# Optimization experiments

Measured on AMD Instinct MI355X. Metric: run time of the kernel, lower is better.

## Reference

```python
import jax, jax.numpy as jnp
import numpy as np

EPS = 1e-05


def setup_inputs() -> dict:
    key = jax.random.key(0)
    ks = jax.random.split(key, 4)
    B, N, D, H, E = 16, 8192, 128, 64, 64
    x = jax.random.normal(ks[0], (B, N, D), dtype=jnp.float32)
    ln_w = jnp.ones((D,), jnp.float32)
    ln_b = jnp.zeros((D,), jnp.float32)
    Wl = jax.random.normal(ks[1], (D, H), dtype=jnp.float32) / np.sqrt(D)
    bl = jnp.zeros((H,), jnp.float32)
    Wr = jax.random.normal(ks[2], (D, H), dtype=jnp.float32) / np.sqrt(D)
    br = jnp.zeros((H,), jnp.float32)
    Wo = jax.random.normal(ks[3], (H, E), dtype=jnp.float32) / np.sqrt(H)
    bo = jnp.zeros((E,), jnp.float32)
    return {"x": x, "ln_w": ln_w, "ln_b": ln_b, "Wl": Wl, "bl": bl,
            "Wr": Wr, "br": br, "Wo": Wo, "bo": bo}


def _layernorm(x, w, b):
    mu = jnp.mean(x, axis=-1, keepdims=True)
    var = jnp.mean(jnp.square(x - mu), axis=-1, keepdims=True)
    return (x - mu) * jax.lax.rsqrt(var + EPS) * w + b


def reference(x, ln_w, ln_b, Wl, bl, Wr, br, Wo, bo):
    # x: [B, N, D]
    xn = _layernorm(x, ln_w, ln_b)
    left = xn @ Wl + bl    # [B, N, H]
    right = xn @ Wr + br   # [B, N, H]
    # Original: einsum('b i d, b j d -> b i j d').mean(dim=1).
    # Identical math without the O(N^2) tensor: mean over i factors out of
    # the product since left[b,i,d]*right[b,j,d] is separable in i.
    outer = left.mean(axis=1)[:, None, :] * right  # [B, N, H]
    return outer @ Wo + bo  # [B, N, E]
```

## Files before the change

### kernel.cpp

```cpp
#include <hip/hip_runtime.h>
#include <math.h>

#define B_  16
#define N_  8192
#define D_  128
#define H_  64
#define E_  64
#define EPSLN 1e-5f

typedef __attribute__((ext_vector_type(8))) short short8;
typedef __attribute__((ext_vector_type(4))) float f32x4;

#define WSB_COL 0
#define WSB_MT  8192
#define WSB_T   270336
#define WSB_C   274432

static __device__ __forceinline__ unsigned short f2bf(float f) {
    union { float f; unsigned u; } c; c.f = f;
    unsigned u = c.u;
    return (unsigned short)((u + 0x7FFFu + ((u >> 16) & 1u)) >> 16);
}

__global__ __launch_bounds__(256) void k_stats(const float* __restrict__ x,
                                               float* __restrict__ colacc) {
    __shared__ float xs[64 * 132];
    __shared__ float mul[64], rsl[64], red[128];
    int b = blockIdx.y, t = threadIdx.x;
    int rowbase = blockIdx.x * 64;
    size_t gbase = (size_t)(b * N_ + rowbase) * 32;

    const float4* x4 = (const float4*)x;
#pragma unroll
    for (int k = 0; k < 8; ++k) {
        int idx = t + 256 * k;
        int row = idx >> 5, c4 = idx & 31;
        *(float4*)&xs[row * 132 + c4 * 4] = x4[gbase + idx];
    }
    __syncthreads();

    {
        int r = t >> 2, q = t & 3;
        float s = 0.f, s2 = 0.f;
#pragma unroll
        for (int i = 0; i < 8; ++i) {
            float4 v = *(const float4*)&xs[r * 132 + q * 32 + i * 4];
            s  += (v.x + v.y) + (v.z + v.w);
            s2 += (v.x * v.x + v.y * v.y) + (v.z * v.z + v.w * v.w);
        }
        s  += __shfl_xor(s, 1, 64);  s  += __shfl_xor(s, 2, 64);
        s2 += __shfl_xor(s2, 1, 64); s2 += __shfl_xor(s2, 2, 64);
        if (q == 0) {
            float mu  = s * (1.f / D_);
            float var = s2 * (1.f / D_) - mu * mu;
            mul[r] = mu;
            rsl[r] = rsqrtf(var + EPSLN);
        }
    }
    __syncthreads();

    int c = t & 127, hh = t >> 7;
    float acc = 0.f;
#pragma unroll 8
    for (int i = 0; i < 32; ++i) {
        int r = hh * 32 + i;
        acc += rsl[r] * (xs[r * 132 + c] - mul[r]);
    }
    if (hh == 1) red[c] = acc;
    __syncthreads();
    if (hh == 0) atomicAdd(&colacc[b * D_ + c], acc + red[c]);
}

__global__ __launch_bounds__(256) void k_combine(const float* __restrict__ colacc,
                                                 const float* __restrict__ ln_w,
                                                 const float* __restrict__ ln_b,
                                                 const float* __restrict__ Wl,
                                                 const float* __restrict__ bl,
                                                 const float* __restrict__ Wr,
                                                 const float* __restrict__ br,
                                                 const float* __restrict__ Wo,
                                                 const float* __restrict__ bo,
                                                 unsigned short* __restrict__ Mt,
                                                 float* __restrict__ Tg,
                                                 float* __restrict__ Cg) {
    int b = blockIdx.y, dblk = blockIdx.x, t = threadIdx.x;
    __shared__ float cm[D_], ml[H_], uu[H_], qq[H_];
    __shared__ float P[H_ * E_];

    if (t < D_) cm[t] = ln_w[t] * colacc[b * D_ + t] * (1.f / N_) + ln_b[t];
    __syncthreads();

    if (t < H_) {
        float a = bl[t], u = 0.f, q = 0.f;
        for (int d = 0; d < D_; ++d) {
            float wr = Wr[d * H_ + t];
            a += cm[d] * Wl[d * H_ + t];
            u += ln_w[d] * wr;
            q += ln_b[d] * wr;
        }
        ml[t] = a; uu[t] = u; qq[t] = q + br[t];
    }
    __syncthreads();

#pragma unroll
    for (int k = 0; k < 16; ++k) {
        int idx = t + 256 * k;
        P[idx] = ml[idx >> 6] * Wo[idx];
    }
    __syncthreads();

    int d  = dblk * 32 + (t >> 3);
    int eo = (t & 7) * 8;
    float a0 = 0, a1 = 0, a2 = 0, a3 = 0, a4 = 0, a5 = 0, a6 = 0, a7 = 0;
    for (int h = 0; h < H_; ++h) {
        float wr = Wr[d * H_ + h];
        const float4* p4 = (const float4*)&P[h * E_ + eo];
        float4 pa = p4[0], pb = p4[1];
        a0 += wr * pa.x; a1 += wr * pa.y; a2 += wr * pa.z; a3 += wr * pa.w;
        a4 += wr * pb.x; a5 += wr * pb.y; a6 += wr * pb.z; a7 += wr * pb.w;
    }
    float wd = ln_w[d];
    size_t mb = (size_t)b * E_ * D_;
    Mt[mb + (size_t)(eo + 0) * D_ + d] = f2bf(wd * a0);
    Mt[mb + (size_t)(eo + 1) * D_ + d] = f2bf(wd * a1);
    Mt[mb + (size_t)(eo + 2) * D_ + d] = f2bf(wd * a2);
    Mt[mb + (size_t)(eo + 3) * D_ + d] = f2bf(wd * a3);
    Mt[mb + (size_t)(eo + 4) * D_ + d] = f2bf(wd * a4);
    Mt[mb + (size_t)(eo + 5) * D_ + d] = f2bf(wd * a5);
    Mt[mb + (size_t)(eo + 6) * D_ + d] = f2bf(wd * a6);
    Mt[mb + (size_t)(eo + 7) * D_ + d] = f2bf(wd * a7);

    if (dblk == 0 && t < E_) {
        float T = 0.f, C = bo[t];
        for (int h = 0; h < H_; ++h) {
            float p = P[h * E_ + t];
            T += uu[h] * p;
            C += qq[h] * p;
        }
        Tg[b * E_ + t] = T;
        Cg[b * E_ + t] = C;
    }
}

__global__ __launch_bounds__(256, 2) void k_gemm(const float* __restrict__ x,
                                                 const unsigned short* __restrict__ Mt,
                                                 const float* __restrict__ Tg,
                                                 const float* __restrict__ Cg,
                                                 float* __restrict__ out) {
    __shared__ short xs[256 * 128];
    __shared__ float mul[256], rsl[256], Tl[E_], Cl[E_];

    int b = blockIdx.y, t = threadIdx.x;
    int rowbase = blockIdx.x * 256;

    if (t < E_) { Tl[t] = Tg[b * E_ + t]; Cl[t] = Cg[b * E_ + t]; }

    {
        const float4* xrow = (const float4*)(x + (size_t)(b * N_ + rowbase + t) * D_);
        float s = 0.f, s2 = 0.f;
        int sw = t & 15;
#pragma unroll
        for (int g = 0; g < 16; ++g) {
            float4 va = xrow[2 * g], vb = xrow[2 * g + 1];
            s  += (va.x + va.y) + (va.z + va.w) + (vb.x + vb.y) + (vb.z + vb.w);
            s2 += (va.x * va.x + va.y * va.y) + (va.z * va.z + va.w * va.w)
                + (vb.x * vb.x + vb.y * vb.y) + (vb.z * vb.z + vb.w * vb.w);
            short8 sv;
            sv[0] = (short)f2bf(va.x); sv[1] = (short)f2bf(va.y);
            sv[2] = (short)f2bf(va.z); sv[3] = (short)f2bf(va.w);
            sv[4] = (short)f2bf(vb.x); sv[5] = (short)f2bf(vb.y);
            sv[6] = (short)f2bf(vb.z); sv[7] = (short)f2bf(vb.w);
            *(short8*)&xs[t * 128 + ((g ^ sw) * 8)] = sv;
        }
        float mu  = s * (1.f / D_);
        float var = s2 * (1.f / D_) - mu * mu;
        mul[t] = mu;
        rsl[t] = rsqrtf(var + EPSLN);
    }
    __syncthreads();

    int wv = t >> 6, lane = t & 63;
    int m16 = lane & 15, quad = lane >> 4;

    f32x4 acc[4][4];
#pragma unroll
    for (int i = 0; i < 4; ++i)
#pragma unroll
        for (int j = 0; j < 4; ++j) acc[i][j] = (f32x4){0.f, 0.f, 0.f, 0.f};

    const unsigned short* Mb = Mt + (size_t)b * E_ * D_;

#pragma unroll
    for (int kc = 0; kc < 4; ++kc) {
        short8 af[4], bf[4];
#pragma unroll
        for (int mt = 0; mt < 4; ++mt) {
            int row = wv * 64 + mt * 16 + m16;
            int g = kc * 4 + quad;
            af[mt] = *(const short8*)&xs[row * 128 + ((g ^ m16) * 8)];
        }
#pragma unroll
        for (int nt = 0; nt < 4; ++nt) {
            bf[nt] = *(const short8*)(Mb + (size_t)(nt * 16 + m16) * D_ + kc * 32 + quad * 8);
        }
#pragma unroll
        for (int mt = 0; mt < 4; ++mt)
#pragma unroll
            for (int nt = 0; nt < 4; ++nt)
                acc[mt][nt] = __builtin_amdgcn_mfma_f32_16x16x32_bf16(
                    af[mt], bf[nt], acc[mt][nt], 0, 0, 0);
    }

    size_t outbase = (size_t)(b * N_ + rowbase) * E_;
#pragma unroll
    for (int mt = 0; mt < 4; ++mt) {
        int rb = wv * 64 + mt * 16 + quad * 4;
        float mu0 = mul[rb + 0], rs0 = rsl[rb + 0];
        float mu1 = mul[rb + 1], rs1 = rsl[rb + 1];
        float mu2 = mul[rb + 2], rs2 = rsl[rb + 2];
        float mu3 = mul[rb + 3], rs3 = rsl[rb + 3];
#pragma unroll
        for (int nt = 0; nt < 4; ++nt) {
            int col = nt * 16 + m16;
            float Tc = Tl[col], Cc = Cl[col];
            float* o = out + outbase + (size_t)rb * E_ + col;
            o[0 * E_] = rs0 * (acc[mt][nt][0] - mu0 * Tc) + Cc;
            o[1 * E_] = rs1 * (acc[mt][nt][1] - mu1 * Tc) + Cc;
            o[2 * E_] = rs2 * (acc[mt][nt][2] - mu2 * Tc) + Cc;
            o[3 * E_] = rs3 * (acc[mt][nt][3] - mu3 * Tc) + Cc;
        }
    }
}

extern "C" void kernel_launch(void* const* d_in, const int* in_sizes, int n_in,
                              void* d_out, int out_size, void* d_ws, size_t ws_size,
                              hipStream_t stream) {
    const float* x    = (const float*)d_in[0];
    const float* ln_w = (const float*)d_in[1];
    const float* ln_b = (const float*)d_in[2];
    const float* Wl   = (const float*)d_in[3];
    const float* bl   = (const float*)d_in[4];
    const float* Wr   = (const float*)d_in[5];
    const float* br   = (const float*)d_in[6];
    const float* Wo   = (const float*)d_in[7];
    const float* bo   = (const float*)d_in[8];
    float* out = (float*)d_out;
    char* ws   = (char*)d_ws;

    float*          colacc = (float*)(ws + WSB_COL);
    unsigned short* Mt     = (unsigned short*)(ws + WSB_MT);
    float*          Tg     = (float*)(ws + WSB_T);
    float*          Cg     = (float*)(ws + WSB_C);

    hipMemsetAsync(colacc, 0, B_ * D_ * sizeof(float), stream);

    k_stats<<<dim3(N_ / 64, B_), 256, 0, stream>>>(x, colacc);
    k_combine<<<dim3(4, B_), 256, 0, stream>>>(colacc, ln_w, ln_b, Wl, bl, Wr,
                                               br, Wo, bo, Mt, Tg, Cg);
    k_gemm<<<dim3(N_ / 256, B_), 256, 0, stream>>>(x, Mt, Tg, Cg, out);
}
```

Measured before the change: 144.1 us.

## Fuse stats, combine and GEMM into one persistent kernel with grid barriers

Replaces the three-kernel pipeline with a single 256-block kernel that reads x once, converts it to bf16, and keeps one 256-row tile in LDS while spilling the other to a bf16 workspace buffer. Per-block column partials replace the atomic accumulation. Two software grid barriers sequence the weight-combine step and the MFMA GEMM, so x no longer needs a second fp32 read and two launches are removed. The cost is reliance on all 256 blocks being co-resident, a spin barrier with a bailout that could silently break correctness, and column sums now computed from bf16-rounded x.

```diff
diff --git a/kernel.cpp b/kernel.cpp
--- a/kernel.cpp
+++ b/kernel.cpp
@@ -7,179 +7,92 @@
 #define H_  64
 #define E_  64
 #define EPSLN 1e-5f
+#define NBLK 256u
 
 typedef __attribute__((ext_vector_type(8))) short short8;
 typedef __attribute__((ext_vector_type(4))) float f32x4;
 
-#define WSB_COL 0
-#define WSB_MT  8192
-#define WSB_T   270336
-#define WSB_C   274432
+#define WSB_PART 0
+#define WSB_MT   131072
+#define WSB_T    393216
+#define WSB_C    397312
+#define WSB_BAR  401408
+#define WSB_XB   409600
 
 static __device__ __forceinline__ unsigned short f2bf(float f) {
     union { float f; unsigned u; } c; c.f = f;
     unsigned u = c.u;
     return (unsigned short)((u + 0x7FFFu + ((u >> 16) & 1u)) >> 16);
 }
-
-__global__ __launch_bounds__(256) void k_stats(const float* __restrict__ x,
-                                               float* __restrict__ colacc) {
-    __shared__ float xs[64 * 132];
-    __shared__ float mul[64], rsl[64], red[128];
-    int b = blockIdx.y, t = threadIdx.x;
-    int rowbase = blockIdx.x * 64;
-    size_t gbase = (size_t)(b * N_ + rowbase) * 32;
-
-    const float4* x4 = (const float4*)x;
-#pragma unroll
-    for (int k = 0; k < 8; ++k) {
-        int idx = t + 256 * k;
-        int row = idx >> 5, c4 = idx & 31;
-        *(float4*)&xs[row * 132 + c4 * 4] = x4[gbase + idx];
-    }
-    __syncthreads();
-
-    {
-        int r = t >> 2, q = t & 3;
-        float s = 0.f, s2 = 0.f;
-#pragma unroll
-        for (int i = 0; i < 8; ++i) {
-            float4 v = *(const float4*)&xs[r * 132 + q * 32 + i * 4];
-            s  += (v.x + v.y) + (v.z + v.w);
-            s2 += (v.x * v.x + v.y * v.y) + (v.z * v.z + v.w * v.w);
-        }
-        s  += __shfl_xor(s, 1, 64);  s  += __shfl_xor(s, 2, 64);
-        s2 += __shfl_xor(s2, 1, 64); s2 += __shfl_xor(s2, 2, 64);
-        if (q == 0) {
-            float mu  = s * (1.f / D_);
-            float var = s2 * (1.f / D_) - mu * mu;
-            mul[r] = mu;
-            rsl[r] = rsqrtf(var + EPSLN);
-        }
-    }
-    __syncthreads();
-
-    int c = t & 127, hh = t >> 7;
-    float acc = 0.f;
-#pragma unroll 8
-    for (int i = 0; i < 32; ++i) {
-        int r = hh * 32 + i;
-        acc += rsl[r] * (xs[r * 132 + c] - mul[r]);
-    }
-    if (hh == 1) red[c] = acc;
-    __syncthreads();
-    if (hh == 0) atomicAdd(&colacc[b * D_ + c], acc + red[c]);
-}
-
-__global__ __launch_bounds__(256) void k_combine(const float* __restrict__ colacc,
-                                                 const float* __restrict__ ln_w,
-                                                 const float* __restrict__ ln_b,
-                                                 const float* __restrict__ Wl,
-                                                 const float* __restrict__ bl,
-                                                 const float* __restrict__ Wr,
-                                                 const float* __restrict__ br,
-                                                 const float* __restrict__ Wo,
-                                                 const float* __restrict__ bo,
-                                                 unsigned short* __restrict__ Mt,
-                                                 float* __restrict__ Tg,
-                                                 float* __restrict__ Cg) {
-    int b = blockIdx.y, dblk = blockIdx.x, t = threadIdx.x;
-    __shared__ float cm[D_], ml[H_], uu[H_], qq[H_];
-    __shared__ float P[H_ * E_];
-
-    if (t < D_) cm[t] = ln_w[t] * colacc[b * D_ + t] * (1.f / N_) + ln_b[t];
-    __syncthreads();
-
-    if (t < H_) {
-        float a = bl[t], u = 0.f, q = 0.f;
-        for (int d = 0; d < D_; ++d) {
-            float wr = Wr[d * H_ + t];
-            a += cm[d] * Wl[d * H_ + t];
-            u += ln_w[d] * wr;
-            q += ln_b[d] * wr;
-        }
-        ml[t] = a; uu[t] = u; qq[t] = q + br[t];
-    }
-    __syncthreads();
-
-#pragma unroll
-    for (int k = 0; k < 16; ++k) {
-        int idx = t + 256 * k;
-        P[idx] = ml[idx >> 6] * Wo[idx];
-    }
-    __syncthreads();
-
-    int d  = dblk * 32 + (t >> 3);
-    int eo = (t & 7) * 8;
-    float a0 = 0, a1 = 0, a2 = 0, a3 = 0, a4 = 0, a5 = 0, a6 = 0, a7 = 0;
-    for (int h = 0; h < H_; ++h) {
-        float wr = Wr[d * H_ + h];
-        const float4* p4 = (const float4*)&P[h * E_ + eo];
-        float4 pa = p4[0], pb = p4[1];
-        a0 += wr * pa.x; a1 += wr * pa.y; a2 += wr * pa.z; a3 += wr * pa.w;
-        a4 += wr * pb.x; a5 += wr * pb.y; a6 += wr * pb.z; a7 += wr * pb.w;
-    }
-    float wd = ln_w[d];
-    size_t mb = (size_t)b * E_ * D_;
-    Mt[mb + (size_t)(eo + 0) * D_ + d] = f2bf(wd * a0);
-    Mt[mb + (size_t)(eo + 1) * D_ + d] = f2bf(wd * a1);
-    Mt[mb + (size_t)(eo + 2) * D_ + d] = f2bf(wd * a2);
-    Mt[mb + (size_t)(eo + 3) * D_ + d] = f2bf(wd * a3);
-    Mt[mb + (size_t)(eo + 4) * D_ + d] = f2bf(wd * a4);
-    Mt[mb + (size_t)(eo + 5) * D_ + d] = f2bf(wd * a5);
-    Mt[mb + (size_t)(eo + 6) * D_ + d] = f2bf(wd * a6);
-    Mt[mb + (size_t)(eo + 7) * D_ + d] = f2bf(wd * a7);
-
-    if (dblk == 0 && t < E_) {
-        float T = 0.f, C = bo[t];
-        for (int h = 0; h < H_; ++h) {
-            float p = P[h * E_ + t];
-            T += uu[h] * p;
-            C += qq[h] * p;
-        }
-        Tg[b * E_ + t] = T;
-        Cg[b * E_ + t] = C;
-    }
-}
-
-__global__ __launch_bounds__(256, 2) void k_gemm(const float* __restrict__ x,
-                                                 const unsigned short* __restrict__ Mt,
-                                                 const float* __restrict__ Tg,
-                                                 const float* __restrict__ Cg,
-                                                 float* __restrict__ out) {
-    __shared__ short xs[256 * 128];
-    __shared__ float mul[256], rsl[256], Tl[E_], Cl[E_];
-
-    int b = blockIdx.y, t = threadIdx.x;
-    int rowbase = blockIdx.x * 256;
-
-    if (t < E_) { Tl[t] = Tg[b * E_ + t]; Cl[t] = Cg[b * E_ + t]; }
-
-    {
-        const float4* xrow = (const float4*)(x + (size_t)(b * N_ + rowbase + t) * D_);
-        float s = 0.f, s2 = 0.f;
-        int sw = t & 15;
-#pragma unroll
-        for (int g = 0; g < 16; ++g) {
-            float4 va = xrow[2 * g], vb = xrow[2 * g + 1];
-            s  += (va.x + va.y) + (va.z + va.w) + (vb.x + vb.y) + (vb.z + vb.w);
-            s2 += (va.x * va.x + va.y * va.y) + (va.z * va.z + va.w * va.w)
-                + (vb.x * vb.x + vb.y * vb.y) + (vb.z * vb.z + vb.w * vb.w);
-            short8 sv;
-            sv[0] = (short)f2bf(va.x); sv[1] = (short)f2bf(va.y);
-            sv[2] = (short)f2bf(va.z); sv[3] = (short)f2bf(va.w);
-            sv[4] = (short)f2bf(vb.x); sv[5] = (short)f2bf(vb.y);
-            sv[6] = (short)f2bf(vb.z); sv[7] = (short)f2bf(vb.w);
-            *(short8*)&xs[t * 128 + ((g ^ sw) * 8)] = sv;
-        }
-        float mu  = s * (1.f / D_);
-        float var = s2 * (1.f / D_) - mu * mu;
-        mul[t] = mu;
-        rsl[t] = rsqrtf(var + EPSLN);
-    }
-    __syncthreads();
-
-    int wv = t >> 6, lane = t & 63;
+static __device__ __forceinline__ float bf2f(short s) {
+    union { unsigned u; float f; } c;
+    c.u = ((unsigned)(unsigned short)s) << 16;
+    return c.f;
+}
+
+static __device__ __forceinline__ void gridbar(unsigned* bar, unsigned target) {
+    __syncthreads();
+    if (threadIdx.x == 0) {
+        __threadfence();
+        atomicAdd(bar, 1u);
+        int spins = 0;
+        while (atomicAdd(bar, 0u) < target) {
+            __builtin_amdgcn_s_sleep(32);
+            if (++spins > (1 << 15)) break;
+        }
+        __threadfence();
+    }
+    __syncthreads();
+}
+
+static __device__ __forceinline__ void stage_rows(const float* __restrict__ xrows,
+                                                  int t, short* xs,
+                                                  float* muA, float* rsA) {
+    const float4* xrow = (const float4*)(xrows + (size_t)t * D_);
+    float s = 0.f, s2 = 0.f;
+    int sw = t & 15;
+#pragma unroll
+    for (int g = 0; g < 16; ++g) {
+        float4 va = xrow[2 * g], vb = xrow[2 * g + 1];
+        s  += (va.x + va.y) + (va.z + va.w) + (vb.x + vb.y) + (vb.z + vb.w);
+        s2 += (va.x * va.x + va.y * va.y) + (va.z * va.z + va.w * va.w)
+            + (vb.x * vb.x + vb.y * vb.y) + (vb.z * vb.z + vb.w * vb.w);
+        short8 sv;
+        sv[0] = (short)f2bf(va.x); sv[1] = (short)f2bf(va.y);
+        sv[2] = (short)f2bf(va.z); sv[3] = (short)f2bf(va.w);
+        sv[4] = (short)f2bf(vb.x); sv[5] = (short)f2bf(vb.y);
+        sv[6] = (short)f2bf(vb.z); sv[7] = (short)f2bf(vb.w);
+        *(short8*)&xs[t * 128 + ((g ^ sw) * 8)] = sv;
+    }
+    float mu  = s * (1.f / D_);
+    float var = s2 * (1.f / D_) - mu * mu;
+    muA[t] = mu;
+    rsA[t] = rsqrtf(var + EPSLN);
+}
+
+static __device__ __forceinline__ void colsum_pass(const short* xs,
+                                                   const float* muA, const float* rsA,
+                                                   int t, float* ca, float* srm) {
+    int rc = t >> 4, cg = t & 15;
+#pragma unroll
+    for (int i = 0; i < 16; ++i) {
+        int r = rc * 16 + i;
+        float rs = rsA[r];
+        *srm += rs * muA[r];
+        short8 v = *(const short8*)&xs[r * 128 + ((cg ^ (r & 15)) << 3)];
+        ca[0] += rs * bf2f(v[0]); ca[1] += rs * bf2f(v[1]);
+        ca[2] += rs * bf2f(v[2]); ca[3] += rs * bf2f(v[3]);
+        ca[4] += rs * bf2f(v[4]); ca[5] += rs * bf2f(v[5]);
+        ca[6] += rs * bf2f(v[6]); ca[7] += rs * bf2f(v[7]);
+    }
+}
+
+static __device__ __forceinline__ void mfma_tile(const short* xs,
+                                                 const unsigned short* __restrict__ Mb,
+                                                 const float* muA, const float* rsA,
+                                                 const float* Tl, const float* Cl,
+                                                 float* __restrict__ outp,
+                                                 int wv, int lane) {
     int m16 = lane & 15, quad = lane >> 4;
 
     f32x4 acc[4][4];
@@ -187,8 +100,6 @@
     for (int i = 0; i < 4; ++i)
 #pragma unroll
         for (int j = 0; j < 4; ++j) acc[i][j] = (f32x4){0.f, 0.f, 0.f, 0.f};
-
-    const unsigned short* Mb = Mt + (size_t)b * E_ * D_;
 
 #pragma unroll
     for (int kc = 0; kc < 4; ++kc) {
@@ -211,25 +122,156 @@
                     af[mt], bf[nt], acc[mt][nt], 0, 0, 0);
     }
 
-    size_t outbase = (size_t)(b * N_ + rowbase) * E_;
 #pragma unroll
     for (int mt = 0; mt < 4; ++mt) {
         int rb = wv * 64 + mt * 16 + quad * 4;
-        float mu0 = mul[rb + 0], rs0 = rsl[rb + 0];
-        float mu1 = mul[rb + 1], rs1 = rsl[rb + 1];
-        float mu2 = mul[rb + 2], rs2 = rsl[rb + 2];
-        float mu3 = mul[rb + 3], rs3 = rsl[rb + 3];
+        float mu0 = muA[rb + 0], rs0 = rsA[rb + 0];
+        float mu1 = muA[rb + 1], rs1 = rsA[rb + 1];
+        float mu2 = muA[rb + 2], rs2 = rsA[rb + 2];
+        float mu3 = muA[rb + 3], rs3 = rsA[rb + 3];
 #pragma unroll
         for (int nt = 0; nt < 4; ++nt) {
             int col = nt * 16 + m16;
             float Tc = Tl[col], Cc = Cl[col];
-            float* o = out + outbase + (size_t)rb * E_ + col;
+            float* o = outp + (size_t)rb * E_ + col;
             o[0 * E_] = rs0 * (acc[mt][nt][0] - mu0 * Tc) + Cc;
             o[1 * E_] = rs1 * (acc[mt][nt][1] - mu1 * Tc) + Cc;
             o[2 * E_] = rs2 * (acc[mt][nt][2] - mu2 * Tc) + Cc;
             o[3 * E_] = rs3 * (acc[mt][nt][3] - mu3 * Tc) + Cc;
         }
     }
+}
+
+__global__ __launch_bounds__(256, 2) void k_fused(
+    const float* __restrict__ x,
+    const float* __restrict__ ln_w, const float* __restrict__ ln_b,
+    const float* __restrict__ Wl,   const float* __restrict__ bl,
+    const float* __restrict__ Wr,   const float* __restrict__ br,
+    const float* __restrict__ Wo,   const float* __restrict__ bo,
+    float* __restrict__ partial, unsigned short* __restrict__ Mt,
+    float* __restrict__ Tg, float* __restrict__ Cg,
+    unsigned* __restrict__ bar, unsigned short* __restrict__ xb,
+    float* __restrict__ out)
+{
+    __shared__ short xs[256 * 128];
+    __shared__ float muA[256], rsA[256], muB[256], rsB[256];
+    __shared__ float red[16 * 128];
+    __shared__ float cm[D_], mlv[H_], uu[H_], qq[H_];
+    __shared__ float Tl[E_], Cl[E_];
+
+    int by = blockIdx.y, bx = blockIdx.x, t = threadIdx.x;
+    int rowbase = bx * 512;
+    const float* xrows = x + (size_t)(by * N_ + rowbase) * D_;
+    unsigned short* xbB = xb + (size_t)(by * 16 + bx) * (256 * 128);
+
+    float ca[8] = {0.f, 0.f, 0.f, 0.f, 0.f, 0.f, 0.f, 0.f};
+    float srm = 0.f;
+
+    stage_rows(xrows + (size_t)256 * D_, t, xs, muB, rsB);
+    __syncthreads();
+    colsum_pass(xs, muB, rsB, t, ca, &srm);
+    {
+        const short8* s8 = (const short8*)xs;
+        short8* d8 = (short8*)xbB;
+#pragma unroll
+        for (int i = 0; i < 16; ++i) d8[t + 256 * i] = s8[t + 256 * i];
+    }
+    __syncthreads();
+
+    stage_rows(xrows, t, xs, muA, rsA);
+    __syncthreads();
+    colsum_pass(xs, muA, rsA, t, ca, &srm);
+
+    {
+        int rc = t >> 4, cg = t & 15;
+#pragma unroll
+        for (int j = 0; j < 8; ++j) red[rc * 128 + cg * 8 + j] = ca[j] - srm;
+    }
+    __syncthreads();
+    if (t < 128) {
+        float v = 0.f;
+#pragma unroll
+        for (int rc = 0; rc < 16; ++rc) v += red[rc * 128 + t];
+        partial[(size_t)(by * 16 + bx) * D_ + t] = v;
+    }
+
+    gridbar(&bar[0], NBLK);
+
+    if (bx < 4) {
+        if (t < D_) {
+            float sacc = 0.f;
+#pragma unroll
+            for (int j = 0; j < 16; ++j)
+                sacc += partial[(size_t)(by * 16 + j) * D_ + t];
+            cm[t] = ln_w[t] * sacc * (1.f / N_) + ln_b[t];
+        }
+        __syncthreads();
+        if (t < H_) {
+            float a = bl[t], u = 0.f, q = 0.f;
+            for (int d = 0; d < D_; ++d) {
+                float wr = Wr[d * H_ + t];
+                a += cm[d] * Wl[d * H_ + t];
+                u += ln_w[d] * wr;
+                q += ln_b[d] * wr;
+            }
+            mlv[t] = a; uu[t] = u; qq[t] = q + br[t];
+        }
+        __syncthreads();
+        {
+            int d  = bx * 32 + (t >> 3);
+            int eo = (t & 7) * 8;
+            float a0 = 0, a1 = 0, a2 = 0, a3 = 0, a4 = 0, a5 = 0, a6 = 0, a7 = 0;
+            for (int h = 0; h < H_; ++h) {
+                float coef = Wr[d * H_ + h] * mlv[h];
+                const float4* wo4 = (const float4*)&Wo[h * E_ + eo];
+                float4 pa = wo4[0], pb = wo4[1];
+                a0 += coef * pa.x; a1 += coef * pa.y; a2 += coef * pa.z; a3 += coef * pa.w;
+                a4 += coef * pb.x; a5 += coef * pb.y; a6 += coef * pb.z; a7 += coef * pb.w;
+            }
+            float wd = ln_w[d];
+            size_t mb = (size_t)by * E_ * D_;
+            Mt[mb + (size_t)(eo + 0) * D_ + d] = f2bf(wd * a0);
+            Mt[mb + (size_t)(eo + 1) * D_ + d] = f2bf(wd * a1);
+            Mt[mb + (size_t)(eo + 2) * D_ + d] = f2bf(wd * a2);
+            Mt[mb + (size_t)(eo + 3) * D_ + d] = f2bf(wd * a3);
+            Mt[mb + (size_t)(eo + 4) * D_ + d] = f2bf(wd * a4);
+            Mt[mb + (size_t)(eo + 5) * D_ + d] = f2bf(wd * a5);
+            Mt[mb + (size_t)(eo + 6) * D_ + d] = f2bf(wd * a6);
+            Mt[mb + (size_t)(eo + 7) * D_ + d] = f2bf(wd * a7);
+        }
+        if (bx == 0 && t < E_) {
+            float T = 0.f, C = bo[t];
+            for (int h = 0; h < H_; ++h) {
+                float p = mlv[h] * Wo[h * E_ + t];
+                T += uu[h] * p;
+                C += qq[h] * p;
+            }
+            Tg[by * E_ + t] = T;
+            Cg[by * E_ + t] = C;
+        }
+    }
+
+    gridbar(&bar[1], NBLK);
+
+    if (t < E_) { Tl[t] = Tg[by * E_ + t]; Cl[t] = Cg[by * E_ + t]; }
+    __syncthreads();
+
+    int wv = t >> 6, lane = t & 63;
+    const unsigned short* Mb = Mt + (size_t)by * E_ * D_;
+    size_t ob = (size_t)(by * N_ + rowbase) * E_;
+
+    mfma_tile(xs, Mb, muA, rsA, Tl, Cl, out + ob, wv, lane);
+
+    __syncthreads();
+    {
+        const short8* s8 = (const short8*)xbB;
+        short8* d8 = (short8*)xs;
+#pragma unroll
+        for (int i = 0; i < 16; ++i) d8[t + 256 * i] = s8[t + 256 * i];
+    }
+    __syncthreads();
+
+    mfma_tile(xs, Mb, muB, rsB, Tl, Cl, out + ob + (size_t)256 * E_, wv, lane);
 }
 
 extern "C" void kernel_launch(void* const* d_in, const int* in_sizes, int n_in,
@@ -247,15 +289,16 @@
     float* out = (float*)d_out;
     char* ws   = (char*)d_ws;
 
-    float*          colacc = (float*)(ws + WSB_COL);
-    unsigned short* Mt     = (unsigned short*)(ws + WSB_MT);
-    float*          Tg     = (float*)(ws + WSB_T);
-    float*          Cg     = (float*)(ws + WSB_C);
-
-    hipMemsetAsync(colacc, 0, B_ * D_ * sizeof(float), stream);
-
-    k_stats<<<dim3(N_ / 64, B_), 256, 0, stream>>>(x, colacc);
-    k_combine<<<dim3(4, B_), 256, 0, stream>>>(colacc, ln_w, ln_b, Wl, bl, Wr,
-                                               br, Wo, bo, Mt, Tg, Cg);
-    k_gemm<<<dim3(N_ / 256, B_), 256, 0, stream>>>(x, Mt, Tg, Cg, out);
-}
+    float*          partial = (float*)(ws + WSB_PART);
+    unsigned short* Mt      = (unsigned short*)(ws + WSB_MT);
+    float*          Tg      = (float*)(ws + WSB_T);
+    float*          Cg      = (float*)(ws + WSB_C);
+    unsigned*       bar     = (unsigned*)(ws + WSB_BAR);
+    unsigned short* xb      = (unsigned short*)(ws + WSB_XB);
+
+    hipMemsetAsync(bar, 0, 2 * sizeof(unsigned), stream);
+
+    k_fused<<<dim3(16, 16), dim3(256), 0, stream>>>(
+        x, ln_w, ln_b, Wl, bl, Wr, br, Wo, bo,
+        partial, Mt, Tg, Cg, bar, xb, out);
+}
```

New measurement: 187.1 us. 29.8% more time.

## Cache row stats, replace atomics with partial sums, coalesce GEMM x loads

Applied to the files above, without the earlier changes.

k_stats now writes per-row mean and rsqrt to a workspace buffer and stores per-block column partials instead of doing atomicAdds. This removes the memset and the atomic contention, and k_combine reduces the partials itself. k_gemm3 reads the cached stats instead of recomputing them, and loads x with coalesced float4 accesses across threads instead of one row per thread. The cost is extra workspace traffic for the partials and the stats, plus a longer serial reduction loop in k_combine.

```diff
diff --git a/kernel.cpp b/kernel.cpp
--- a/kernel.cpp
+++ b/kernel.cpp
@@ -9,12 +9,14 @@
 #define EPSLN 1e-5f
 
 typedef __attribute__((ext_vector_type(8))) short short8;
+typedef __attribute__((ext_vector_type(4))) short short4v;
 typedef __attribute__((ext_vector_type(4))) float f32x4;
 
-#define WSB_COL 0
-#define WSB_MT  8192
-#define WSB_T   270336
-#define WSB_C   274432
+#define WSB_PART 0
+#define WSB_MT   1048576
+#define WSB_T    1310720
+#define WSB_C    1314816
+#define WSB_MURS 1318912
 
 static __device__ __forceinline__ unsigned short f2bf(float f) {
     union { float f; unsigned u; } c; c.f = f;
@@ -23,7 +25,8 @@
 }
 
 __global__ __launch_bounds__(256) void k_stats(const float* __restrict__ x,
-                                               float* __restrict__ colacc) {
+                                               float* __restrict__ partial,
+                                               float2* __restrict__ murs) {
     __shared__ float xs[64 * 132];
     __shared__ float mul[64], rsl[64], red[128];
     int b = blockIdx.y, t = threadIdx.x;
@@ -59,6 +62,11 @@
     }
     __syncthreads();
 
+    if (t < 64) {
+        float2 mr; mr.x = mul[t]; mr.y = rsl[t];
+        murs[(size_t)b * N_ + rowbase + t] = mr;
+    }
+
     int c = t & 127, hh = t >> 7;
     float acc = 0.f;
 #pragma unroll 8
@@ -68,10 +76,11 @@
     }
     if (hh == 1) red[c] = acc;
     __syncthreads();
-    if (hh == 0) atomicAdd(&colacc[b * D_ + c], acc + red[c]);
-}
-
-__global__ __launch_bounds__(256) void k_combine(const float* __restrict__ colacc,
+    if (hh == 0)
+        partial[((size_t)b * 128 + blockIdx.x) * D_ + c] = acc + red[c];
+}
+
+__global__ __launch_bounds__(256) void k_combine(const float* __restrict__ partial,
                                                  const float* __restrict__ ln_w,
                                                  const float* __restrict__ ln_b,
                                                  const float* __restrict__ Wl,
@@ -86,8 +95,17 @@
     int b = blockIdx.y, dblk = blockIdx.x, t = threadIdx.x;
     __shared__ float cm[D_], ml[H_], uu[H_], qq[H_];
     __shared__ float P[H_ * E_];
-
-    if (t < D_) cm[t] = ln_w[t] * colacc[b * D_ + t] * (1.f / N_) + ln_b[t];
+    __shared__ float red2[256];
+
+    {
+        int d = t & 127, hhf = t >> 7;
+        float sacc = 0.f;
+        for (int j = hhf * 64; j < hhf * 64 + 64; ++j)
+            sacc += partial[((size_t)b * 128 + j) * D_ + d];
+        red2[t] = sacc;
+    }
+    __syncthreads();
+    if (t < D_) cm[t] = ln_w[t] * (red2[t] + red2[t + 128]) * (1.f / N_) + ln_b[t];
     __syncthreads();
 
     if (t < H_) {
@@ -142,40 +160,39 @@
     }
 }
 
-__global__ __launch_bounds__(256, 2) void k_gemm(const float* __restrict__ x,
-                                                 const unsigned short* __restrict__ Mt,
-                                                 const float* __restrict__ Tg,
-                                                 const float* __restrict__ Cg,
-                                                 float* __restrict__ out) {
+__global__ __launch_bounds__(256, 2) void k_gemm3(const float* __restrict__ x,
+                                                  const float2* __restrict__ murs,
+                                                  const unsigned short* __restrict__ Mt,
+                                                  const float* __restrict__ Tg,
+                                                  const float* __restrict__ Cg,
+                                                  float* __restrict__ out) {
     __shared__ short xs[256 * 128];
-    __shared__ float mul[256], rsl[256], Tl[E_], Cl[E_];
-
-    int b = blockIdx.y, t = threadIdx.x;
-    int rowbase = blockIdx.x * 256;
+    __shared__ float muL[256], rsL[256], Tl[E_], Cl[E_];
+
+    int b = blockIdx.y, bx = blockIdx.x, t = threadIdx.x;
+    int rowbase = bx * 256;
 
     if (t < E_) { Tl[t] = Tg[b * E_ + t]; Cl[t] = Cg[b * E_ + t]; }
-
     {
-        const float4* xrow = (const float4*)(x + (size_t)(b * N_ + rowbase + t) * D_);
-        float s = 0.f, s2 = 0.f;
-        int sw = t & 15;
-#pragma unroll
-        for (int g = 0; g < 16; ++g) {
-            float4 va = xrow[2 * g], vb = xrow[2 * g + 1];
-            s  += (va.x + va.y) + (va.z + va.w) + (vb.x + vb.y) + (vb.z + vb.w);
-            s2 += (va.x * va.x + va.y * va.y) + (va.z * va.z + va.w * va.w)
-                + (vb.x * vb.x + vb.y * vb.y) + (vb.z * vb.z + vb.w * vb.w);
-            short8 sv;
-            sv[0] = (short)f2bf(va.x); sv[1] = (short)f2bf(va.y);
-            sv[2] = (short)f2bf(va.z); sv[3] = (short)f2bf(va.w);
-            sv[4] = (short)f2bf(vb.x); sv[5] = (short)f2bf(vb.y);
-            sv[6] = (short)f2bf(vb.z); sv[7] = (short)f2bf(vb.w);
-            *(short8*)&xs[t * 128 + ((g ^ sw) * 8)] = sv;
-        }
-        float mu  = s * (1.f / D_);
-        float var = s2 * (1.f / D_) - mu * mu;
-        mul[t] = mu;
-        rsl[t] = rsqrtf(var + EPSLN);
+        float2 mr = murs[(size_t)b * N_ + rowbase + t];
+        muL[t] = mr.x; rsL[t] = mr.y;
+    }
+
+    const float4* x4 = (const float4*)x;
+    size_t gbase = (size_t)(b * N_ + rowbase) * 32;
+
+    for (int kk = 0; kk < 4; ++kk) {
+#pragma unroll
+        for (int k = 0; k < 8; ++k) {
+            int idx = t + 256 * (kk * 8 + k);
+            int row = idx >> 5, c4 = idx & 31;
+            float4 v = x4[gbase + idx];
+            short4v sv;
+            sv[0] = (short)f2bf(v.x); sv[1] = (short)f2bf(v.y);
+            sv[2] = (short)f2bf(v.z); sv[3] = (short)f2bf(v.w);
+            int g2 = c4 >> 1, half = c4 & 1;
+            *(short4v*)&xs[row * 128 + ((g2 ^ (row & 15)) << 3) + (half << 2)] = sv;
+        }
     }
     __syncthreads();
 
@@ -215,10 +232,10 @@
 #pragma unroll
     for (int mt = 0; mt < 4; ++mt) {
         int rb = wv * 64 + mt * 16 + quad * 4;
-        float mu0 = mul[rb + 0], rs0 = rsl[rb + 0];
-        float mu1 = mul[rb + 1], rs1 = rsl[rb + 1];
-        float mu2 = mul[rb + 2], rs2 = rsl[rb + 2];
-        float mu3 = mul[rb + 3], rs3 = rsl[rb + 3];
+        float mu0 = muL[rb + 0], rs0 = rsL[rb + 0];
+        float mu1 = muL[rb + 1], rs1 = rsL[rb + 1];
+        float mu2 = muL[rb + 2], rs2 = rsL[rb + 2];
+        float mu3 = muL[rb + 3], rs3 = rsL[rb + 3];
 #pragma unroll
         for (int nt = 0; nt < 4; ++nt) {
             int col = nt * 16 + m16;
@@ -247,15 +264,16 @@
     float* out = (float*)d_out;
     char* ws   = (char*)d_ws;
 
-    float*          colacc = (float*)(ws + WSB_COL);
-    unsigned short* Mt     = (unsigned short*)(ws + WSB_MT);
-    float*          Tg     = (float*)(ws + WSB_T);
-    float*          Cg     = (float*)(ws + WSB_C);
-
-    hipMemsetAsync(colacc, 0, B_ * D_ * sizeof(float), stream);
-
-    k_stats<<<dim3(N_ / 64, B_), 256, 0, stream>>>(x, colacc);
-    k_combine<<<dim3(4, B_), 256, 0, stream>>>(colacc, ln_w, ln_b, Wl, bl, Wr,
-                                               br, Wo, bo, Mt, Tg, Cg);
-    k_gemm<<<dim3(N_ / 256, B_), 256, 0, stream>>>(x, Mt, Tg, Cg, out);
-}
+    float*          partial = (float*)(ws + WSB_PART);
+    unsigned short* Mt      = (unsigned short*)(ws + WSB_MT);
+    float*          Tg      = (float*)(ws + WSB_T);
+    float*          Cg      = (float*)(ws + WSB_C);
+    float2*         murs    = (float2*)(ws + WSB_MURS);
+
+    k_stats<<<dim3(128, 16), dim3(256), 0, stream>>>(x, partial, murs);
+
+    k_combine<<<dim3(4, 16), dim3(256), 0, stream>>>(partial, ln_w, ln_b, Wl, bl,
+                                                     Wr, br, Wo, bo, Mt, Tg, Cg);
+
+    k_gemm3<<<dim3(32, 16), dim3(256), 0, stream>>>(x, murs, Mt, Tg, Cg, out);
+}
```

After: 153.1 us. 1.06x slower.
